# Performance work log

Measured on AMD Instinct MI355X. Metric: run time of the kernel, lower is better.

Reference implementation:

```python
import jax, jax.numpy as jnp
import numpy as np


def setup_inputs() -> dict:
    key = jax.random.key(0)
    ks = jax.random.split(key, 7)
    B, T, IN_F = 16384, 64, 48
    F = 32          # feature_size = len(INTERACTIVE_LIST)
    H = 128         # embedding_hidden_size
    TF, TH = T * F, T * H
    scale1 = 1.0 / np.sqrt(TF)
    scale2 = 1.0 / np.sqrt(TH)
    return {
        "x": jax.random.normal(ks[0], (B, T, IN_F), dtype=jnp.float32),
        "W1": jax.random.normal(ks[1], (TF, TH), dtype=jnp.float32) * scale1,
        "b1": jax.random.normal(ks[2], (TH,), dtype=jnp.float32) * scale1,
        "W2": jax.random.normal(ks[3], (TH, TF), dtype=jnp.float32) * scale2,
        "b2": jax.random.normal(ks[4], (TF,), dtype=jnp.float32) * scale2,
        "weight": jax.random.normal(ks[5], (T, F), dtype=jnp.float32),
        "bias": jax.random.normal(ks[6], (F,), dtype=jnp.float32) * (1.0 / np.sqrt(T)),
        "sample_index": jnp.arange(F, dtype=jnp.int32),
    }


def reference(x, W1, b1, W2, b2, weight, bias, sample_index):
    # x: [B, T, IN_F]; gather interactive feature columns -> [B, T, F]
    B = x.shape[0]
    T, F = weight.shape
    xs = jnp.take(x, sample_index, axis=2)            # [B, T, F]
    # pass_linear=True path: MLP on flattened time*feature vector
    h = jax.nn.relu(xs.reshape(B, T * F) @ W1 + b1)   # [B, T*H]; dropout = identity (eval)
    out = (h @ W2 + b2).reshape(B, T, F)              # [B, T, F]
    # vectorized form of the per-sample loop: sum over time of elementwise mul
    emb = jnp.einsum("btf,tf->bf", out, weight) + bias  # [B, F]
    return emb
```

## Files before the change

kernel.cpp:

```cpp
#include <hip/hip_runtime.h>
#include <hip/hip_bf16.h>

#define BATCH 16384
#define TT    64
#define INF   48
#define FF    32
#define TFD   2048
#define THD   8192

typedef __attribute__((ext_vector_type(8))) short bf16x8;
typedef __attribute__((ext_vector_type(4))) short bf16x4;
typedef __attribute__((ext_vector_type(4))) short short4v;
typedef __attribute__((ext_vector_type(4))) float f32x4;

#define SCHED __builtin_amdgcn_sched_barrier(0)
#define VMW(n) asm volatile("s_waitcnt vmcnt(" #n ")" ::: "memory")

__device__ inline void gload_lds16(const void* g, void* l) {
  __builtin_amdgcn_global_load_lds((const __attribute__((address_space(1))) void*)g,
                                   (__attribute__((address_space(3))) void*)l, 16, 0, 0);
}

__device__ inline f32x4 mfma16x16x16_bf16(bf16x4 a, bf16x4 b, f32x4 c) {
#if __has_builtin(__builtin_amdgcn_mfma_f32_16x16x16bf16_1k)
  return __builtin_amdgcn_mfma_f32_16x16x16bf16_1k(a, b, c, 0, 0, 0);
#else
  asm("v_mfma_f32_16x16x16_bf16 %0, %1, %2, %0" : "+v"(c) : "v"(a), "v"(b));
  return c;
#endif
}

__device__ inline short f32_to_bf16_bits(float x) {
  __hip_bfloat16 h = __float2bfloat16(x);
  return *reinterpret_cast<short*>(&h);
}


__global__ void gather_cast_frag(const float* __restrict__ x, const int* __restrict__ sidx,
                                 __hip_bfloat16* __restrict__ xsf) {
  __shared__ int sx[FF];
  if (threadIdx.x < FF) sx[threadIdx.x] = sidx[threadIdx.x];
  __syncthreads();
  const int b64 = blockIdx.x >> 2;
  const int tq  = blockIdx.x & 3;
  for (int it = 0; it < 16; ++it) {
    const int slot = (tq * 16 + it) * 256 + threadIdx.x;
    const int t  = slot >> 8;
    const int bi = (slot >> 6) & 3;
    const int l  = slot & 63;
    const int lo = l & 15, hi = l >> 4;
    const int row = b64 * 64 + bi * 16 + lo;
    const float* rp = x + ((size_t)row * TT + t) * INF;
    bf16x8 v;
    #pragma unroll
    for (int j = 0; j < 8; ++j) v[j] = f32_to_bf16_bits(rp[sx[hi * 8 + j]]);
    *(bf16x8*)(xsf + ((size_t)b64 * 16384 + slot) * 8) = v;
  }
}

__global__ void transpose_w1(const float* __restrict__ W1, __hip_bfloat16* __restrict__ W1t) {
  __shared__ float tile[64][65];
  const int k0 = blockIdx.x * 64;
  const int n0 = blockIdx.y * 64;
  const int tx = threadIdx.x & 63, ty = threadIdx.x >> 6;
  for (int r = ty; r < 64; r += 4)
    tile[r][tx] = W1[(size_t)(k0 + r) * THD + n0 + tx];
  __syncthreads();
  const int rn = threadIdx.x >> 4;
  const int kq = (threadIdx.x & 15) * 4;
  for (int rr = rn; rr < 64; rr += 16) {
    short4v v;
    #pragma unroll
    for (int i = 0; i < 4; ++i) v[i] = f32_to_bf16_bits(tile[kq + i][rr]);
    *(short4v*)(W1t + (size_t)(n0 + rr) * TFD + k0 + kq) = v;
  }
}

__global__ void make_w2eff(const float* __restrict__ W2, const float* __restrict__ b2,
                           const float* __restrict__ weight, const float* __restrict__ bias,
                           __hip_bfloat16* __restrict__ w2t, float* __restrict__ beff) {
  const int n = blockIdx.x * 8 + (threadIdx.x >> 5);
  const int f = threadIdx.x & 31;
  const float* wr = W2 + (size_t)n * TFD;
  float s = 0.f;
  #pragma unroll 8
  for (int t = 0; t < TT; ++t) s += wr[t * FF + f] * weight[t * FF + f];
  w2t[(size_t)f * THD + n] = __float2bfloat16(s);
  if (blockIdx.x == 0 && threadIdx.x < FF) {
    float sb = bias[f];
    for (int t = 0; t < TT; ++t) sb += b2[t * FF + f] * weight[t * FF + f];
    beff[f] = sb;
  }
}


__device__ inline void stage_w16(char* buf, const __hip_bfloat16* __restrict__ w1t,
                                 int n0, int k0, int wid, int l) {
  const int sub = l >> 3;
  const int c   = (l & 7) ^ sub;
  const int h   = c >> 2, kc = c & 3;
  const int r0  = wid * 8 + sub;
  const __hip_bfloat16* gw = w1t + (size_t)(n0 + 2 * r0 + h) * TFD + k0 + kc * 8;
  gload_lds16(gw, buf + wid * 1024);
}

__device__ inline void stage_x16(char* bufX, const char* __restrict__ xg, int t, int wid, int l) {
  const int g = wid >> 2, bi = wid & 3;
  const char* src = xg + (size_t)g * 262144 + ((t * 4 + bi) * 1024) + l * 16;
  gload_lds16(src, bufX + wid * 1024);
}

__global__ __launch_bounds__(1024, 4) void gemm_fused(
    const __hip_bfloat16* __restrict__ xsf,
    const __hip_bfloat16* __restrict__ w1t,
    const float* __restrict__ b1,
    const __hip_bfloat16* __restrict__ w2t,
    float* __restrict__ partial)
{
  __shared__ __align__(16) char lds[131072];
  const int tid = threadIdx.x;
  const int wid = tid >> 6, l = tid & 63;
  const int wn = wid >> 2, wb = wid & 3;
  const int lo = l & 15, hi = l >> 4;
  const int rl = lo >> 1;
  const int cofs = (((((lo & 1) << 2) | hi) ^ rl) << 4);
  const int strip = blockIdx.x & 7;
  const int bt = blockIdx.x >> 3;
  const int b0 = bt * 256;

  const int wbase = ((wn << 5) + rl) * 128 + cofs;
  const int xoffr = 16384 + (wb << 12) + l * 16;
  const char* xg  = (const char*)xsf + (size_t)(bt * 4) * 262144;

  f32x4 acc2[2][4];
  #pragma unroll
  for (int fi = 0; fi < 2; ++fi)
    #pragma unroll
    for (int bi = 0; bi < 4; ++bi) { f32x4 z = {0.f,0.f,0.f,0.f}; acc2[fi][bi] = z; }

  for (int s = 0; s < 4; ++s) {
    const int n0 = strip * 1024 + s * 256;

    f32x4 acc[4][4];
    #pragma unroll
    for (int mi = 0; mi < 4; ++mi)
      #pragma unroll
      for (int bi = 0; bi < 4; ++bi) { f32x4 z = {0.f,0.f,0.f,0.f}; acc[mi][bi] = z; }

    stage_w16(lds, w1t, n0, 0, wid, l);
    stage_x16(lds + 16384, xg, 0, wid, l);
    SCHED;
    stage_w16(lds + 32768, w1t, n0, 32, wid, l);
    stage_x16(lds + 32768 + 16384, xg, 1, wid, l);
    SCHED;
    VMW(2); SCHED;
    __builtin_amdgcn_s_barrier(); SCHED;

    for (int t = 0; t < 64; ++t) {
      char* buf = lds + (size_t)(t & 3) * 32768;
      if (t <= 61) {
        char* nbuf = lds + (size_t)((t + 2) & 3) * 32768;
        stage_w16(nbuf, w1t, n0, (t + 2) * 32, wid, l);
        stage_x16(nbuf + 16384, xg, t + 2, wid, l);
      }
      SCHED;
      bf16x8 wf0 = *(const bf16x8*)(buf + wbase);
      bf16x8 wf1 = *(const bf16x8*)(buf + wbase + 1024);
      bf16x8 wf2 = *(const bf16x8*)(buf + wbase + 2048);
      bf16x8 wf3 = *(const bf16x8*)(buf + wbase + 3072);
      bf16x8 xf0 = *(const bf16x8*)(buf + xoffr);
      bf16x8 xf1 = *(const bf16x8*)(buf + xoffr + 1024);
      bf16x8 xf2 = *(const bf16x8*)(buf + xoffr + 2048);
      bf16x8 xf3 = *(const bf16x8*)(buf + xoffr + 3072);
      __builtin_amdgcn_s_setprio(1);
      acc[0][0] = __builtin_amdgcn_mfma_f32_16x16x32_bf16(wf0, xf0, acc[0][0], 0, 0, 0);
      acc[0][1] = __builtin_amdgcn_mfma_f32_16x16x32_bf16(wf0, xf1, acc[0][1], 0, 0, 0);
      acc[0][2] = __builtin_amdgcn_mfma_f32_16x16x32_bf16(wf0, xf2, acc[0][2], 0, 0, 0);
      acc[0][3] = __builtin_amdgcn_mfma_f32_16x16x32_bf16(wf0, xf3, acc[0][3], 0, 0, 0);
      acc[1][0] = __builtin_amdgcn_mfma_f32_16x16x32_bf16(wf1, xf0, acc[1][0], 0, 0, 0);
      acc[1][1] = __builtin_amdgcn_mfma_f32_16x16x32_bf16(wf1, xf1, acc[1][1], 0, 0, 0);
      acc[1][2] = __builtin_amdgcn_mfma_f32_16x16x32_bf16(wf1, xf2, acc[1][2], 0, 0, 0);
      acc[1][3] = __builtin_amdgcn_mfma_f32_16x16x32_bf16(wf1, xf3, acc[1][3], 0, 0, 0);
      acc[2][0] = __builtin_amdgcn_mfma_f32_16x16x32_bf16(wf2, xf0, acc[2][0], 0, 0, 0);
      acc[2][1] = __builtin_amdgcn_mfma_f32_16x16x32_bf16(wf2, xf1, acc[2][1], 0, 0, 0);
      acc[2][2] = __builtin_amdgcn_mfma_f32_16x16x32_bf16(wf2, xf2, acc[2][2], 0, 0, 0);
      acc[2][3] = __builtin_amdgcn_mfma_f32_16x16x32_bf16(wf2, xf3, acc[2][3], 0, 0, 0);
      acc[3][0] = __builtin_amdgcn_mfma_f32_16x16x32_bf16(wf3, xf0, acc[3][0], 0, 0, 0);
      acc[3][1] = __builtin_amdgcn_mfma_f32_16x16x32_bf16(wf3, xf1, acc[3][1], 0, 0, 0);
      acc[3][2] = __builtin_amdgcn_mfma_f32_16x16x32_bf16(wf3, xf2, acc[3][2], 0, 0, 0);
      acc[3][3] = __builtin_amdgcn_mfma_f32_16x16x32_bf16(wf3, xf3, acc[3][3], 0, 0, 0);
      __builtin_amdgcn_s_setprio(0);
      SCHED;
      if (t <= 61)      { VMW(2); }
      else if (t == 62) { VMW(0); }
      SCHED;
      __builtin_amdgcn_s_barrier(); SCHED;
    }

    #pragma unroll
    for (int mi = 0; mi < 4; ++mi) {
      const int nbase = n0 + (wn << 6) + (mi << 4);
      const float4 b1v = *(const float4*)(b1 + nbase + (hi << 2));
      bf16x4 p[4];
      #pragma unroll
      for (int bi = 0; bi < 4; ++bi) {
        bf16x4 pk;
        #pragma unroll
        for (int j = 0; j < 4; ++j) {
          float v = acc[mi][bi][j] + ((const float*)&b1v)[j];
          v = v > 0.f ? v : 0.f;
          pk[j] = f32_to_bf16_bits(v);
        }
        p[bi] = pk;
      }
      bf16x4 a2[2];
      #pragma unroll
      for (int fi = 0; fi < 2; ++fi)
        a2[fi] = *(const bf16x4*)(w2t + (size_t)(fi * 16 + lo) * THD + nbase + (hi << 2));
      #pragma unroll
      for (int fi = 0; fi < 2; ++fi)
        #pragma unroll
        for (int bi = 0; bi < 4; ++bi)
          acc2[fi][bi] = mfma16x16x16_bf16(a2[fi], p[bi], acc2[fi][bi]);
    }
  }

  float* sm = (float*)lds;
  __syncthreads();
  if (wn != 0) {
    float* slab = sm + (size_t)(wn - 1) * 8192;
    #pragma unroll
    for (int fi = 0; fi < 2; ++fi)
      #pragma unroll
      for (int bi = 0; bi < 4; ++bi)
        *(f32x4*)(slab + ((wb << 6) + (bi << 4) + lo) * 32 + fi * 16 + (hi << 2)) = acc2[fi][bi];
  }
  __syncthreads();
  if (wn == 0) {
    #pragma unroll
    for (int fi = 0; fi < 2; ++fi)
      #pragma unroll
      for (int bi = 0; bi < 4; ++bi) {
        const int off = ((wb << 6) + (bi << 4) + lo) * 32 + fi * 16 + (hi << 2);
        f32x4 v = acc2[fi][bi];
        v = v + *(const f32x4*)(sm + off);
        v = v + *(const f32x4*)(sm + 8192 + off);
        v = v + *(const f32x4*)(sm + 16384 + off);
        *(f32x4*)(partial + ((size_t)strip * BATCH + b0 + (wb << 6) + (bi << 4) + lo) * FF + fi * 16 + (hi << 2)) = v;
      }
  }
}

__global__ void reduce_partial(const float* __restrict__ partial, const float* __restrict__ beff,
                               float* __restrict__ out) {
  const int idx = blockIdx.x * 256 + threadIdx.x;
  float s = beff[idx & 31];
  #pragma unroll
  for (int c = 0; c < 8; ++c) s += partial[(size_t)c * BATCH * FF + idx];
  out[idx] = s;
}


extern "C" void kernel_launch(void* const* d_in, const int* in_sizes, int n_in,
                              void* d_out, int out_size, void* d_ws, size_t ws_size,
                              hipStream_t stream) {
  const float* x      = (const float*)d_in[0];
  const float* W1     = (const float*)d_in[1];
  const float* b1     = (const float*)d_in[2];
  const float* W2     = (const float*)d_in[3];
  const float* b2     = (const float*)d_in[4];
  const float* weight = (const float*)d_in[5];
  const float* bias   = (const float*)d_in[6];
  const int*   sidx   = (const int*)d_in[7];

  char* ws = (char*)d_ws;
  __hip_bfloat16* xsf  = (__hip_bfloat16*)ws;
  __hip_bfloat16* w1t  = (__hip_bfloat16*)(ws + 67108864);
  __hip_bfloat16* w2t  = (__hip_bfloat16*)(ws + 100663296);
  float*          beff = (float*)(ws + 101187584);
  float*          part = (float*)(ws + 101188608);

  hipLaunchKernelGGL(gather_cast_frag, dim3(1024), dim3(256), 0, stream, x, sidx, xsf);
  hipLaunchKernelGGL(transpose_w1, dim3(32, 128), dim3(256), 0, stream, W1, w1t);
  hipLaunchKernelGGL(make_w2eff,   dim3(1024),    dim3(256), 0, stream, W2, b2, weight, bias, w2t, beff);
  hipLaunchKernelGGL(gemm_fused,   dim3(512),     dim3(1024), 0, stream, xsf, w1t, b1, w2t, part);
  hipLaunchKernelGGL(reduce_partial, dim3(2048),  dim3(256), 0, stream, part, beff, (float*)d_out);
}
```

Baseline: 661.2 us.

## Load x fragments directly from global into registers, bypassing LDS staging

The x operand is no longer staged through LDS. Each wave now loads its x fragments straight from global memory into double-buffered registers (xfA/xfB), prefetched two steps ahead, while W1 still goes through a 4-deep LDS ring that shrinks to 16KB stages. This removes the x LDS writes and reads and cuts LDS use from 128KB to 96KB. In exchange it raises register pressure and adds per-wave global loads with different vmcnt accounting, and any x reuse across the four wn wave groups now comes from cache instead of a shared LDS copy.

```diff
diff --git a/kernel.cpp b/kernel.cpp
--- a/kernel.cpp
+++ b/kernel.cpp
@@ -104,10 +104,45 @@
   gload_lds16(gw, buf + wid * 1024);
 }
 
-__device__ inline void stage_x16(char* bufX, const char* __restrict__ xg, int t, int wid, int l) {
-  const int g = wid >> 2, bi = wid & 3;
-  const char* src = xg + (size_t)g * 262144 + ((t * 4 + bi) * 1024) + l * 16;
-  gload_lds16(src, bufX + wid * 1024);
+__device__ __forceinline__ void k_iter(char* lds, int t, int n0,
+    const char* __restrict__ xbase, const __hip_bfloat16* __restrict__ w1t,
+    f32x4 (&acc)[4][4], bf16x8 (&xfu)[4],
+    int wbase, int wid, int l) {
+  if (t <= 61) stage_w16(lds + (size_t)((t + 2) & 3) * 16384, w1t, n0, (t + 2) * 32, wid, l);
+  SCHED;
+  const char* buf = lds + (size_t)(t & 3) * 16384;
+  bf16x8 wf0 = *(const bf16x8*)(buf + wbase);
+  bf16x8 wf1 = *(const bf16x8*)(buf + wbase + 1024);
+  bf16x8 wf2 = *(const bf16x8*)(buf + wbase + 2048);
+  bf16x8 wf3 = *(const bf16x8*)(buf + wbase + 3072);
+  __builtin_amdgcn_s_setprio(1);
+  acc[0][0] = __builtin_amdgcn_mfma_f32_16x16x32_bf16(wf0, xfu[0], acc[0][0], 0, 0, 0);
+  acc[0][1] = __builtin_amdgcn_mfma_f32_16x16x32_bf16(wf0, xfu[1], acc[0][1], 0, 0, 0);
+  acc[0][2] = __builtin_amdgcn_mfma_f32_16x16x32_bf16(wf0, xfu[2], acc[0][2], 0, 0, 0);
+  acc[0][3] = __builtin_amdgcn_mfma_f32_16x16x32_bf16(wf0, xfu[3], acc[0][3], 0, 0, 0);
+  acc[1][0] = __builtin_amdgcn_mfma_f32_16x16x32_bf16(wf1, xfu[0], acc[1][0], 0, 0, 0);
+  acc[1][1] = __builtin_amdgcn_mfma_f32_16x16x32_bf16(wf1, xfu[1], acc[1][1], 0, 0, 0);
+  acc[1][2] = __builtin_amdgcn_mfma_f32_16x16x32_bf16(wf1, xfu[2], acc[1][2], 0, 0, 0);
+  acc[1][3] = __builtin_amdgcn_mfma_f32_16x16x32_bf16(wf1, xfu[3], acc[1][3], 0, 0, 0);
+  acc[2][0] = __builtin_amdgcn_mfma_f32_16x16x32_bf16(wf2, xfu[0], acc[2][0], 0, 0, 0);
+  acc[2][1] = __builtin_amdgcn_mfma_f32_16x16x32_bf16(wf2, xfu[1], acc[2][1], 0, 0, 0);
+  acc[2][2] = __builtin_amdgcn_mfma_f32_16x16x32_bf16(wf2, xfu[2], acc[2][2], 0, 0, 0);
+  acc[2][3] = __builtin_amdgcn_mfma_f32_16x16x32_bf16(wf2, xfu[3], acc[2][3], 0, 0, 0);
+  acc[3][0] = __builtin_amdgcn_mfma_f32_16x16x32_bf16(wf3, xfu[0], acc[3][0], 0, 0, 0);
+  acc[3][1] = __builtin_amdgcn_mfma_f32_16x16x32_bf16(wf3, xfu[1], acc[3][1], 0, 0, 0);
+  acc[3][2] = __builtin_amdgcn_mfma_f32_16x16x32_bf16(wf3, xfu[2], acc[3][2], 0, 0, 0);
+  acc[3][3] = __builtin_amdgcn_mfma_f32_16x16x32_bf16(wf3, xfu[3], acc[3][3], 0, 0, 0);
+  __builtin_amdgcn_s_setprio(0);
+  if (t <= 61) {
+    #pragma unroll
+    for (int bi = 0; bi < 4; ++bi)
+      xfu[bi] = *(const bf16x8*)(xbase + ((t + 2) * 4 + bi) * 1024);
+  }
+  SCHED;
+  if (t <= 61)      { VMW(5); }
+  else if (t == 62) { VMW(0); }
+  SCHED;
+  __builtin_amdgcn_s_barrier(); SCHED;
 }
 
 __global__ __launch_bounds__(1024, 4) void gemm_fused(
@@ -117,7 +152,7 @@
     const __hip_bfloat16* __restrict__ w2t,
     float* __restrict__ partial)
 {
-  __shared__ __align__(16) char lds[131072];
+  __shared__ __align__(16) char lds[98304];
   const int tid = threadIdx.x;
   const int wid = tid >> 6, l = tid & 63;
   const int wn = wid >> 2, wb = wid & 3;
@@ -129,8 +164,7 @@
   const int b0 = bt * 256;
 
   const int wbase = ((wn << 5) + rl) * 128 + cofs;
-  const int xoffr = 16384 + (wb << 12) + l * 16;
-  const char* xg  = (const char*)xsf + (size_t)(bt * 4) * 262144;
+  const char* xbase = (const char*)xsf + ((size_t)(bt * 4 + wb) * 16384 + l) * 16;
 
   f32x4 acc2[2][4];
   #pragma unroll
@@ -147,54 +181,21 @@
       #pragma unroll
       for (int bi = 0; bi < 4; ++bi) { f32x4 z = {0.f,0.f,0.f,0.f}; acc[mi][bi] = z; }
 
-    stage_w16(lds, w1t, n0, 0, wid, l);
-    stage_x16(lds + 16384, xg, 0, wid, l);
+    bf16x8 xfA[4], xfB[4];
+    stage_w16(lds,         w1t, n0, 0,  wid, l); SCHED;
+    stage_w16(lds + 16384, w1t, n0, 32, wid, l); SCHED;
+    #pragma unroll
+    for (int bi = 0; bi < 4; ++bi) xfA[bi] = *(const bf16x8*)(xbase + (0 * 4 + bi) * 1024);
     SCHED;
-    stage_w16(lds + 32768, w1t, n0, 32, wid, l);
-    stage_x16(lds + 32768 + 16384, xg, 1, wid, l);
+    #pragma unroll
+    for (int bi = 0; bi < 4; ++bi) xfB[bi] = *(const bf16x8*)(xbase + (1 * 4 + bi) * 1024);
     SCHED;
-    VMW(2); SCHED;
+    VMW(9); SCHED;
     __builtin_amdgcn_s_barrier(); SCHED;
 
-    for (int t = 0; t < 64; ++t) {
-      char* buf = lds + (size_t)(t & 3) * 32768;
-      if (t <= 61) {
-        char* nbuf = lds + (size_t)((t + 2) & 3) * 32768;
-        stage_w16(nbuf, w1t, n0, (t + 2) * 32, wid, l);
-        stage_x16(nbuf + 16384, xg, t + 2, wid, l);
-      }
-      SCHED;
-      bf16x8 wf0 = *(const bf16x8*)(buf + wbase);
-      bf16x8 wf1 = *(const bf16x8*)(buf + wbase + 1024);
-      bf16x8 wf2 = *(const bf16x8*)(buf + wbase + 2048);
-      bf16x8 wf3 = *(const bf16x8*)(buf + wbase + 3072);
-      bf16x8 xf0 = *(const bf16x8*)(buf + xoffr);
-      bf16x8 xf1 = *(const bf16x8*)(buf + xoffr + 1024);
-      bf16x8 xf2 = *(const bf16x8*)(buf + xoffr + 2048);
-      bf16x8 xf3 = *(const bf16x8*)(buf + xoffr + 3072);
-      __builtin_amdgcn_s_setprio(1);
-      acc[0][0] = __builtin_amdgcn_mfma_f32_16x16x32_bf16(wf0, xf0, acc[0][0], 0, 0, 0);
-      acc[0][1] = __builtin_amdgcn_mfma_f32_16x16x32_bf16(wf0, xf1, acc[0][1], 0, 0, 0);
-      acc[0][2] = __builtin_amdgcn_mfma_f32_16x16x32_bf16(wf0, xf2, acc[0][2], 0, 0, 0);
-      acc[0][3] = __builtin_amdgcn_mfma_f32_16x16x32_bf16(wf0, xf3, acc[0][3], 0, 0, 0);
-      acc[1][0] = __builtin_amdgcn_mfma_f32_16x16x32_bf16(wf1, xf0, acc[1][0], 0, 0, 0);
-      acc[1][1] = __builtin_amdgcn_mfma_f32_16x16x32_bf16(wf1, xf1, acc[1][1], 0, 0, 0);
-      acc[1][2] = __builtin_amdgcn_mfma_f32_16x16x32_bf16(wf1, xf2, acc[1][2], 0, 0, 0);
-      acc[1][3] = __builtin_amdgcn_mfma_f32_16x16x32_bf16(wf1, xf3, acc[1][3], 0, 0, 0);
-      acc[2][0] = __builtin_amdgcn_mfma_f32_16x16x32_bf16(wf2, xf0, acc[2][0], 0, 0, 0);
-      acc[2][1] = __builtin_amdgcn_mfma_f32_16x16x32_bf16(wf2, xf1, acc[2][1], 0, 0, 0);
-      acc[2][2] = __builtin_amdgcn_mfma_f32_16x16x32_bf16(wf2, xf2, acc[2][2], 0, 0, 0);
-      acc[2][3] = __builtin_amdgcn_mfma_f32_16x16x32_bf16(wf2, xf3, acc[2][3], 0, 0, 0);
-      acc[3][0] = __builtin_amdgcn_mfma_f32_16x16x32_bf16(wf3, xf0, acc[3][0], 0, 0, 0);
-      acc[3][1] = __builtin_amdgcn_mfma_f32_16x16x32_bf16(wf3, xf1, acc[3][1], 0, 0, 0);
-      acc[3][2] = __builtin_amdgcn_mfma_f32_16x16x32_bf16(wf3, xf2, acc[3][2], 0, 0, 0);
-      acc[3][3] = __builtin_amdgcn_mfma_f32_16x16x32_bf16(wf3, xf3, acc[3][3], 0, 0, 0);
-      __builtin_amdgcn_s_setprio(0);
-      SCHED;
-      if (t <= 61)      { VMW(2); }
-      else if (t == 62) { VMW(0); }
-      SCHED;
-      __builtin_amdgcn_s_barrier(); SCHED;
+    for (int tt = 0; tt < 64; tt += 2) {
+      k_iter(lds, tt,     n0, xbase, w1t, acc, xfA, wbase, wid, l);
+      k_iter(lds, tt + 1, n0, xbase, w1t, acc, xfB, wbase, wid, l);
     }
 
     #pragma unroll
```

Measured after the change: 772.5 us. +16.8%, slower.
